# Performance work log

Hardware: AMD Instinct MI355X
Metric: run time of the kernel (lower is better)

The kernel has to match this reference:

```python
import jax, jax.numpy as jnp
import numpy as np

EPS = 1e-5

def _batchnorm(x, gamma, beta):
    # x: [N, C, T]; training-mode BN: batch stats over (N, T) per channel
    mean = jnp.mean(x, axis=(0, 2), keepdims=True)
    var = jnp.mean((x - mean) ** 2, axis=(0, 2), keepdims=True)
    xhat = (x - mean) * jax.lax.rsqrt(var + EPS)
    return xhat * gamma[None, :, None] + beta[None, :, None]

def _temporal_shift(x, s):
    # x: [N, C, T], s: [C] learnable per-channel shift (Shift-GCN style)
    # out[n,c,t] = linear interp of x[n,c, t + s[c]], zero outside [0, T)
    N, C, T = x.shape
    pos = jnp.arange(T, dtype=x.dtype)[None, :] + s[:, None]  # [C, T]
    i0f = jnp.floor(pos)
    frac = pos - i0f                                          # [C, T]
    i0 = i0f.astype(jnp.int32)
    i1 = i0 + 1
    v0 = ((i0 >= 0) & (i0 < T)).astype(x.dtype)
    v1 = ((i1 >= 0) & (i1 < T)).astype(x.dtype)
    cidx = jnp.arange(C)[:, None]                             # [C, 1]
    g0 = x[:, cidx, jnp.clip(i0, 0, T - 1)]                   # [N, C, T]
    g1 = x[:, cidx, jnp.clip(i1, 0, T - 1)]
    return g0 * ((1.0 - frac) * v0) + g1 * (frac * v1)

def setup_inputs() -> dict:
    key = jax.random.key(0)
    ks = jax.random.split(key, 5)
    N, T, Cin, Cout = 128, 1024, 256, 256
    x = jax.random.normal(ks[0], (N, T, Cin), dtype=jnp.float32)
    # kaiming_normal fan_out for 1x1 conv: std = sqrt(2 / Cout)
    conv_w = jax.random.normal(ks[1], (Cout, Cin), dtype=jnp.float32) * np.sqrt(2.0 / Cout)
    conv_b = jnp.zeros((Cout,), dtype=jnp.float32)
    shift_in_s = jax.random.uniform(ks[2], (Cin,), dtype=jnp.float32, minval=-1.0, maxval=1.0)
    shift_out_s = jax.random.uniform(ks[3], (Cout,), dtype=jnp.float32, minval=-1.0, maxval=1.0)
    return {
        "x": x,
        "bn1_gamma": jnp.ones((Cin,), jnp.float32),
        "bn1_beta": jnp.zeros((Cin,), jnp.float32),
        "shift_in_s": shift_in_s,
        "conv_w": conv_w,
        "conv_b": conv_b,
        "shift_out_s": shift_out_s,
        "bn2_gamma": jnp.ones((Cout,), jnp.float32),
        "bn2_beta": jnp.zeros((Cout,), jnp.float32),
    }

def reference(x, bn1_gamma, bn1_beta, shift_in_s, conv_w, conv_b, shift_out_s, bn2_gamma, bn2_beta):
    # x: [N, T, C] -> [N, C, T] (permute; trailing singleton W dim elided)
    h = jnp.transpose(x, (0, 2, 1))
    h = _batchnorm(h, bn1_gamma, bn1_beta)
    h = _temporal_shift(h, shift_in_s)
    # 1x1 conv == per-position channel mixing
    h = jnp.einsum("nct,oc->not", h, conv_w) + conv_b[None, :, None]
    h = jax.nn.relu(h)
    h = _temporal_shift(h, shift_out_s)
    h = _batchnorm(h, bn2_gamma, bn2_beta)
    return jnp.transpose(h, (0, 2, 1))  # back to [N, T, C_out]
```

## Files before the change

kernel.cpp:

```cpp
#include <hip/hip_runtime.h>
#include <stddef.h>

typedef __attribute__((ext_vector_type(8))) short short8;
typedef __attribute__((ext_vector_type(4))) float f32x4;
typedef __attribute__((ext_vector_type(4))) int   i32x4;
typedef __attribute__((ext_vector_type(2))) unsigned int u32x2;
typedef unsigned short ushort_t;
typedef unsigned int uint_t;

#define TT 1024
#define NT 131072.0f
#define EPS 1e-5f

__device__ __forceinline__ float bf2f(ushort_t u){
    union { float f; uint_t i; } v; v.i = ((uint_t)u) << 16; return v.f;
}
__device__ __forceinline__ ushort_t f2bf(float f){
    union { float f; uint_t i; } v; v.f = f;
    uint_t r = v.i + 0x7fffu + ((v.i >> 16) & 1u);
    return (ushort_t)(r >> 16);
}
__device__ __forceinline__ uint_t pack2(float lo, float hi){
    return (uint_t)f2bf(lo) | ((uint_t)f2bf(hi) << 16);
}
__device__ __forceinline__ f32x4 ld4bf(const ushort_t* p){
    u32x2 u = *(const u32x2*)p;
    f32x4 r;
    r[0] = bf2f((ushort_t)(u[0] & 0xffffu));
    r[1] = bf2f((ushort_t)(u[0] >> 16));
    r[2] = bf2f((ushort_t)(u[1] & 0xffffu));
    r[3] = bf2f((ushort_t)(u[1] >> 16));
    return r;
}
__device__ __forceinline__ void wave_red(float& v){
    #pragma unroll
    for (int off = 32; off > 0; off >>= 1) v += __shfl_down(v, off);
}

__global__ __launch_bounds__(256) void k_stats1(const float* __restrict__ x,
                                                ushort_t* __restrict__ xb16,
                                                float* __restrict__ psum,
                                                float* __restrict__ psq){
    __shared__ float ls[4][256], lq[4][256];
    const int b = blockIdx.x, tid = threadIdx.x;
    const int c4 = (tid & 63) << 2, rq = tid >> 6;
    const size_t row0 = ((size_t)b << 6) + ((size_t)rq << 4);
    const float* p = x + (row0 << 8) + c4;
    ushort_t* w = xb16 + (row0 << 8) + c4;
    f32x4 s = {0.f,0.f,0.f,0.f}, q = {0.f,0.f,0.f,0.f};
    #pragma unroll 8
    for (int k = 0; k < 16; ++k){
        f32x4 v = *(const f32x4*)&p[(size_t)k << 8];
        u32x2 u; u[0] = pack2(v[0], v[1]); u[1] = pack2(v[2], v[3]);
        *(u32x2*)&w[(size_t)k << 8] = u;
        #pragma unroll
        for (int j = 0; j < 4; ++j){ s[j] += v[j]; q[j] = fmaf(v[j], v[j], q[j]); }
    }
    #pragma unroll
    for (int j = 0; j < 4; ++j){ ls[rq][c4 + j] = s[j]; lq[rq][c4 + j] = q[j]; }
    __syncthreads();
    const int c = tid;
    psum[(size_t)b * 256 + c] = ls[0][c] + ls[1][c] + ls[2][c] + ls[3][c];
    psq [(size_t)b * 256 + c] = lq[0][c] + lq[1][c] + lq[2][c] + lq[3][c];
}

__global__ __launch_bounds__(256) void k_fin1(const float* __restrict__ psum,
                                              const float* __restrict__ psq,
                                              const float* __restrict__ g1,
                                              const float* __restrict__ be1,
                                              const float* __restrict__ sin_,
                                              const float* __restrict__ sout,
                                              float* __restrict__ s1, float* __restrict__ b1,
                                              float* __restrict__ a0i, float* __restrict__ a1i,
                                              int* __restrict__ i1i,
                                              float* __restrict__ a0o, float* __restrict__ a1o,
                                              int* __restrict__ j1o){
    const int c = blockIdx.x, t = threadIdx.x;
    float s = 0.f, q = 0.f;
    #pragma unroll
    for (int i = 0; i < 8; ++i){
        const size_t b = (size_t)(t * 8 + i);
        s += psum[b * 256 + c]; q += psq[b * 256 + c];
    }
    wave_red(s); wave_red(q);
    __shared__ float sm[8];
    const int wv = t >> 6, ln = t & 63;
    if (ln == 0){ sm[wv] = s; sm[4 + wv] = q; }
    __syncthreads();
    if (t == 0){
        float S = sm[0] + sm[1] + sm[2] + sm[3];
        float Q = sm[4] + sm[5] + sm[6] + sm[7];
        float mean = S / NT;
        float var  = Q / NT - mean * mean;
        float rstd = rsqrtf(var + EPS);
        float sc = rstd * g1[c];
        s1[c] = sc;
        b1[c] = be1[c] - mean * sc;
        float sv = sin_[c]; float fi = floorf(sv); float fr = sv - fi;
        a0i[c] = 1.f - fr; a1i[c] = fr; i1i[c] = (int)fi + 1;
        float so = sout[c]; float fo = floorf(so); float fro = so - fo;
        a0o[c] = 1.f - fro; a1o[c] = fro; j1o[c] = (int)fo + 1;
    }
}

__global__ __launch_bounds__(256) void k_wf(const float* __restrict__ W,
                                            const float* __restrict__ s1,
                                            ushort_t* __restrict__ WF){
    const int gid = blockIdx.x * 256 + threadIdx.x;
    const int l = gid & 63, ob = (gid >> 6) & 15, ks = gid >> 10;
    const int row = ob * 16 + (l & 15);
    const int k0  = ks * 32 + (l >> 4) * 8;
    #pragma unroll
    for (int j = 0; j < 8; ++j)
        WF[(size_t)gid * 8 + j] = f2bf(W[(size_t)row * 256 + k0 + j] * s1[k0 + j]);
}

__global__ __launch_bounds__(256) void k_wb(const float* __restrict__ W,
                                            const float* __restrict__ cb,
                                            const float* __restrict__ b1,
                                            const float* __restrict__ a0i,
                                            const float* __restrict__ a1i,
                                            const int* __restrict__ i1i,
                                            float* __restrict__ bias2,
                                            float* __restrict__ corr0,
                                            float* __restrict__ corrT){
    const int o = blockIdx.x, c = threadIdx.x;
    const float w = W[(size_t)o * 256 + c];
    float wb = w * b1[c];
    float c0 = (i1i[c] == 0) ? wb * a0i[c] : 0.f;
    float cT = (i1i[c] == 1) ? wb * a1i[c] : 0.f;
    wave_red(wb); wave_red(c0); wave_red(cT);
    __shared__ float sm[4][3];
    const int wv = c >> 6, ln = c & 63;
    if (ln == 0){ sm[wv][0] = wb; sm[wv][1] = c0; sm[wv][2] = cT; }
    __syncthreads();
    if (c == 0){
        bias2[o] = cb[o] + sm[0][0] + sm[1][0] + sm[2][0] + sm[3][0];
        corr0[o] = sm[0][1] + sm[1][1] + sm[2][1] + sm[3][1];
        corrT[o] = sm[0][2] + sm[1][2] + sm[2][2] + sm[3][2];
    }
}

__device__ __forceinline__ f32x4 bload16(const ushort_t* xp, int g){
    f32x4 r = {0.f,0.f,0.f,0.f};
    if (g >= 0 && g < TT) r = ld4bf(xp + ((size_t)g << 8));
    return r;
}

__global__ __launch_bounds__(256) void k_conv(const ushort_t* __restrict__ xb,
                                              const ushort_t* __restrict__ WF,
                                              const float* __restrict__ bias2,
                                              const float* __restrict__ corr0,
                                              const float* __restrict__ corrT,
                                              const float* __restrict__ a0i,
                                              const float* __restrict__ a1i,
                                              const int* __restrict__ i1i,
                                              ushort_t* __restrict__ Y,
                                              float* __restrict__ SP, float* __restrict__ SQ,
                                              float* __restrict__ SR,
                                              float* __restrict__ FR, float* __restrict__ LR){
    __shared__ __align__(16) ushort_t lds[16384];
    const int tid = threadIdx.x;
    const int n  = blockIdx.x >> 4;
    const int t0 = (blockIdx.x & 15) << 6;
    const int lane = tid & 63, wv = tid >> 6;

    {
        const int c4 = lane << 2;
        const f32x4 a0v = *(const f32x4*)&a0i[c4];
        const f32x4 a1v = *(const f32x4*)&a1i[c4];
        const i32x4 i1v = *(const i32x4*)&i1i[c4];
        const ushort_t* xp = xb + ((size_t)n << 18) + c4;
        const int rt = t0 + (wv << 4);
        f32x4 Bm1 = bload16(xp, rt - 1);
        f32x4 B0  = bload16(xp, rt);
        #pragma unroll 8
        for (int k = 0; k < 16; ++k){
            f32x4 Bp1 = bload16(xp, rt + k + 1);
            f32x4 v;
            #pragma unroll
            for (int j = 0; j < 4; ++j){
                float zl = i1v[j] ? B0[j]  : Bm1[j];
                float zr = i1v[j] ? Bp1[j] : B0[j];
                v[j] = a0v[j] * zl + a1v[j] * zr;
            }
            const int tw = (wv << 4) + k;
            u32x2 w; w[0] = pack2(v[0], v[1]); w[1] = pack2(v[2], v[3]);
            *(u32x2*)&lds[(tw << 8) + (c4 ^ ((tw & 7) << 3))] = w;
            Bm1 = B0; B0 = Bp1;
        }
    }
    __syncthreads();

    const int l15 = lane & 15, lg = lane >> 4;
    f32x4 acc[4][4];
    #pragma unroll
    for (int r = 0; r < 4; ++r)
        #pragma unroll
        for (int q = 0; q < 4; ++q)
            acc[r][q] = (f32x4){0.f, 0.f, 0.f, 0.f};

    const short8* wf8 = (const short8*)WF;
    #pragma unroll
    for (int ks = 0; ks < 8; ++ks){
        short8 aF[4], bF[4];
        #pragma unroll
        for (int r = 0; r < 4; ++r)
            aF[r] = wf8[(ks * 16 + wv * 4 + r) * 64 + lane];
        const int kk = (ks << 5) + (lg << 3);
        #pragma unroll
        for (int q = 0; q < 4; ++q){
            const int t = (q << 4) | l15;
            bF[q] = *(const short8*)&lds[(t << 8) + (kk ^ ((t & 7) << 3))];
        }
        #pragma unroll
        for (int r = 0; r < 4; ++r)
            #pragma unroll
            for (int q = 0; q < 4; ++q)
                acc[r][q] = __builtin_amdgcn_mfma_f32_16x16x32_bf16(aF[r], bF[q], acc[r][q], 0, 0, 0);
    }
    __syncthreads();

    const bool isFirst = (t0 == 0), isLast = (t0 == 960);
    #pragma unroll
    for (int r = 0; r < 4; ++r){
        const int ob = (wv << 6) + (r << 4) + (lg << 2);
        const f32x4 cbv = *(const f32x4*)&bias2[ob];
        f32x4 c0v = {0.f,0.f,0.f,0.f}, cTv = {0.f,0.f,0.f,0.f};
        if (isFirst) c0v = *(const f32x4*)&corr0[ob];
        if (isLast)  cTv = *(const f32x4*)&corrT[ob];
        #pragma unroll
        for (int q = 0; q < 4; ++q){
            const int t = (q << 4) | l15;
            float v[4];
            #pragma unroll
            for (int j = 0; j < 4; ++j){
                float z = acc[r][q][j] + cbv[j];
                if (isFirst && t == 0)  z -= c0v[j];
                if (isLast  && t == 63) z -= cTv[j];
                v[j] = z > 0.f ? z : 0.f;
            }
            u32x2 w; w[0] = pack2(v[0], v[1]); w[1] = pack2(v[2], v[3]);
            *(u32x2*)&lds[(t << 8) + (ob ^ ((t & 7) << 3))] = w;
        }
    }
    __syncthreads();

    u32x2* Yu = (u32x2*)Y;
    const size_t rbase = ((size_t)n << 10) + t0;
    #pragma unroll
    for (int it = 0; it < 16; ++it){
        const int row = (it << 2) + wv;
        u32x2 v = *(const u32x2*)&lds[(row << 8) + ((lane << 2) ^ ((row & 7) << 3))];
        Yu[((rbase + row) << 6) + lane] = v;
    }
    {
        const int o = tid;
        FR[(size_t)blockIdx.x * 256 + o] = bf2f(lds[o]);
        LR[(size_t)blockIdx.x * 256 + o] = bf2f(lds[(63 << 8) + (o ^ 56)]);
    }
    f32x4 P = {0.f,0.f,0.f,0.f}, Q = P, R = P;
    {
        const int o4 = lane << 2;
        const int r0 = wv << 4;
        f32x4 prev = {0.f,0.f,0.f,0.f};
        if (wv > 0) prev = ld4bf(&lds[((r0 - 1) << 8) + (o4 ^ (((r0 - 1) & 7) << 3))]);
        #pragma unroll 8
        for (int k = 0; k < 16; ++k){
            const int t = r0 + k;
            f32x4 y = ld4bf(&lds[(t << 8) + (o4 ^ ((t & 7) << 3))]);
            #pragma unroll
            for (int j = 0; j < 4; ++j){
                P[j] += y[j];
                Q[j] = fmaf(y[j], y[j], Q[j]);
                R[j] = fmaf(prev[j], y[j], R[j]);
            }
            prev = y;
        }
    }
    __syncthreads();
    float* fl = (float*)lds;
    {
        const int o4 = lane << 2;
        *(f32x4*)&fl[wv * 768 + o4]       = P;
        *(f32x4*)&fl[wv * 768 + 256 + o4] = Q;
        *(f32x4*)&fl[wv * 768 + 512 + o4] = R;
    }
    __syncthreads();
    {
        const int o = tid;
        float p = fl[o] + fl[768 + o] + fl[1536 + o] + fl[2304 + o];
        float q = fl[256 + o] + fl[1024 + o] + fl[1792 + o] + fl[2560 + o];
        float r = fl[512 + o] + fl[1280 + o] + fl[2048 + o] + fl[2816 + o];
        const size_t idx = (size_t)blockIdx.x * 256 + o;
        SP[idx] = p; SQ[idx] = q; SR[idx] = r;
    }
}

__global__ __launch_bounds__(256) void k_fin2(const float* __restrict__ SP,
                                              const float* __restrict__ SQ,
                                              const float* __restrict__ SR,
                                              const float* __restrict__ FR,
                                              const float* __restrict__ LR,
                                              const float* __restrict__ g2,
                                              const float* __restrict__ be2,
                                              const float* __restrict__ a0o,
                                              const float* __restrict__ a1o,
                                              const int* __restrict__ j1o,
                                              float* __restrict__ s2, float* __restrict__ b2){
    const int o = blockIdx.x, t = threadIdx.x;
    float P = 0.f, Q = 0.f, R = 0.f, b0p = 0.f, b0q = 0.f, btp = 0.f, btq = 0.f;
    #pragma unroll
    for (int i = 0; i < 8; ++i){
        const int b = t * 8 + i;
        const size_t idx = (size_t)b * 256 + o;
        P += SP[idx]; Q += SQ[idx];
        float r = SR[idx];
        const float fr = FR[idx], lr = LR[idx];
        const int tile = b & 15;
        if (tile > 0) r = fmaf(LR[idx - 256], fr, r);
        R += r;
        if (tile == 0){ b0p += fr; b0q += fr * fr; }
        if (tile == 15){ btp += lr; btq += lr * lr; }
    }
    wave_red(P); wave_red(Q); wave_red(R);
    wave_red(b0p); wave_red(b0q); wave_red(btp); wave_red(btq);
    __shared__ float sm[4][7];
    const int wv = t >> 6, ln = t & 63;
    if (ln == 0){
        sm[wv][0] = P; sm[wv][1] = Q; sm[wv][2] = R;
        sm[wv][3] = b0p; sm[wv][4] = b0q; sm[wv][5] = btp; sm[wv][6] = btq;
    }
    __syncthreads();
    if (t == 0){
        float v[7];
        #pragma unroll
        for (int k = 0; k < 7; ++k)
            v[k] = sm[0][k] + sm[1][k] + sm[2][k] + sm[3][k];
        const float a0 = a0o[o], a1 = a1o[o];
        const int j1 = j1o[o];
        float sz, sq;
        if (j1 == 0){
            sz = a0 * (v[0] - v[5]) + a1 * v[0];
            sq = a0 * a0 * (v[1] - v[6]) + a1 * a1 * v[1] + 2.f * a0 * a1 * v[2];
        } else {
            sz = a0 * v[0] + a1 * (v[0] - v[3]);
            sq = a0 * a0 * v[1] + a1 * a1 * (v[1] - v[4]) + 2.f * a0 * a1 * v[2];
        }
        float mean = sz / NT;
        float var  = sq / NT - mean * mean;
        float rstd = rsqrtf(var + EPS);
        float sc = rstd * g2[o];
        s2[o] = sc;
        b2[o] = be2[o] - mean * sc;
    }
}

__global__ __launch_bounds__(256) void k_out(const ushort_t* __restrict__ Y,
                                             const float* __restrict__ s2,
                                             const float* __restrict__ b2,
                                             const float* __restrict__ a0o,
                                             const float* __restrict__ a1o,
                                             const int* __restrict__ j1o,
                                             float* __restrict__ out){
    const int b = blockIdx.x, tid = threadIdx.x;
    const int n = b >> 3, o4 = (tid & 63) << 2, rq = tid >> 6;
    const int rs = ((b & 7) << 7) + (rq << 5);
    const f32x4 sc = *(const f32x4*)&s2[o4];
    const f32x4 bs = *(const f32x4*)&b2[o4];
    const f32x4 a0 = *(const f32x4*)&a0o[o4];
    const f32x4 a1 = *(const f32x4*)&a1o[o4];
    const i32x4 j1 = *(const i32x4*)&j1o[o4];
    const ushort_t* yb = Y + ((size_t)n << 18) + o4;
    float* ob = out + ((size_t)n << 18) + o4;
    f32x4 ym1 = {0.f,0.f,0.f,0.f};
    if (rs > 0) ym1 = ld4bf(yb + ((size_t)(rs - 1) << 8));
    f32x4 y0 = ld4bf(yb + ((size_t)rs << 8));
    #pragma unroll 8
    for (int k = 0; k < 32; ++k){
        const int t = rs + k;
        f32x4 yp1 = {0.f,0.f,0.f,0.f};
        if (t < 1023) yp1 = ld4bf(yb + ((size_t)(t + 1) << 8));
        f32x4 ov;
        #pragma unroll
        for (int j = 0; j < 4; ++j){
            float zl = j1[j] ? y0[j]  : ym1[j];
            float zr = j1[j] ? yp1[j] : y0[j];
            float z = a0[j] * zl + a1[j] * zr;
            ov[j] = fmaf(z, sc[j], bs[j]);
        }
        *(f32x4*)&ob[(size_t)t << 8] = ov;
        ym1 = y0; y0 = yp1;
    }
}

extern "C" void kernel_launch(void* const* d_in, const int* in_sizes, int n_in,
                              void* d_out, int out_size, void* d_ws, size_t ws_size,
                              hipStream_t stream){
    const float* x    = (const float*)d_in[0];
    const float* g1   = (const float*)d_in[1];
    const float* be1  = (const float*)d_in[2];
    const float* sin_ = (const float*)d_in[3];
    const float* W    = (const float*)d_in[4];
    const float* cb   = (const float*)d_in[5];
    const float* sout = (const float*)d_in[6];
    const float* g2   = (const float*)d_in[7];
    const float* be2  = (const float*)d_in[8];
    float* out = (float*)d_out;

    char* ws = (char*)d_ws;
    ushort_t* Y  = (ushort_t*)ws;
    ushort_t* WF = (ushort_t*)(ws + 67108864);
    float* SP = (float*)(ws + 67239936);
    float* SQ = SP + 524288;
    float* SR = SQ + 524288;
    float* FR = SR + 524288;
    float* LR = FR + 524288;
    float* par = LR + 524288;
    float* s1    = par;         float* b1    = par + 256;
    float* a0i   = par + 512;   float* a1i   = par + 768;
    int*   i1i   = (int*)(par + 1024);
    float* a0o   = par + 1280;  float* a1o   = par + 1536;
    int*   j1o   = (int*)(par + 1792);
    float* s2    = par + 2048;  float* b2    = par + 2304;
    float* bias2 = par + 2560;  float* corr0 = par + 2816;
    float* corrT = par + 3072;
    float* psum = (float*)ws;
    float* psq  = psum + 524288;
    ushort_t* xb16 = (ushort_t*)d_out;

    k_stats1<<<2048, 256, 0, stream>>>(x, xb16, psum, psq);
    k_fin1  <<<256, 256, 0, stream>>>(psum, psq, g1, be1, sin_, sout,
                                      s1, b1, a0i, a1i, i1i, a0o, a1o, j1o);
    k_wf    <<<32, 256, 0, stream>>>(W, s1, WF);
    k_wb    <<<256, 256, 0, stream>>>(W, cb, b1, a0i, a1i, i1i, bias2, corr0, corrT);
    k_conv  <<<2048, 256, 0, stream>>>(xb16, WF, bias2, corr0, corrT,
                                       a0i, a1i, i1i, Y, SP, SQ, SR, FR, LR);
    k_fin2  <<<256, 256, 0, stream>>>(SP, SQ, SR, FR, LR,
                                      g2, be2, a0o, a1o, j1o, s2, b2);
    k_out   <<<1024, 256, 0, stream>>>(Y, s2, b2, a0o, a1o, j1o, out);
}
```

Before: 168.9 us.

## Move input temporal shift into stats kernel and DMA pre-swizzled tile into LDS

The input-side temporal shift interpolation moves from the conv kernel's LDS staging into the first pass over x. That pass now writes a shifted, XOR-swizzled bf16 copy, so k_conv can fill LDS with direct global-to-LDS loads instead of register loads plus ALU work. The shift coefficients are computed in a new tiny kernel launched first, and k_out now uses twice as many blocks with half the rows each. This adds one launch and halo reads of neighbouring rows in the prep pass, in exchange for a leaner conv prologue.

```diff
diff --git a/kernel.cpp b/kernel.cpp
--- a/kernel.cpp
+++ b/kernel.cpp
@@ -36,25 +36,49 @@
     #pragma unroll
     for (int off = 32; off > 0; off >>= 1) v += __shfl_down(v, off);
 }
-
-__global__ __launch_bounds__(256) void k_stats1(const float* __restrict__ x,
-                                                ushort_t* __restrict__ xb16,
-                                                float* __restrict__ psum,
-                                                float* __restrict__ psq){
+__device__ __forceinline__ void dma16(const void* g, void* l){
+    __builtin_amdgcn_global_load_lds(
+        (const __attribute__((address_space(1))) unsigned int*)g,
+        (__attribute__((address_space(3))) unsigned int*)l, 16, 0, 0);
+}
+
+__global__ __launch_bounds__(256) void k_prep(const float* __restrict__ x,
+                                              const float* __restrict__ a0i,
+                                              const float* __restrict__ a1i,
+                                              const int* __restrict__ i1i,
+                                              ushort_t* __restrict__ xs,
+                                              float* __restrict__ psum,
+                                              float* __restrict__ psq){
     __shared__ float ls[4][256], lq[4][256];
     const int b = blockIdx.x, tid = threadIdx.x;
     const int c4 = (tid & 63) << 2, rq = tid >> 6;
     const size_t row0 = ((size_t)b << 6) + ((size_t)rq << 4);
-    const float* p = x + (row0 << 8) + c4;
-    ushort_t* w = xb16 + (row0 << 8) + c4;
+    const int n = (int)(row0 >> 10), rt = (int)(row0 & 1023);
+    const float* xp = x + ((size_t)n << 18) + c4;
+    ushort_t* wp = xs + ((size_t)n << 18);
+    const f32x4 a0v = *(const f32x4*)&a0i[c4];
+    const f32x4 a1v = *(const f32x4*)&a1i[c4];
+    const i32x4 i1v = *(const i32x4*)&i1i[c4];
     f32x4 s = {0.f,0.f,0.f,0.f}, q = {0.f,0.f,0.f,0.f};
+    f32x4 Bm1 = {0.f,0.f,0.f,0.f};
+    if (rt > 0) Bm1 = *(const f32x4*)&xp[(size_t)(rt - 1) << 8];
+    f32x4 B0 = *(const f32x4*)&xp[(size_t)rt << 8];
     #pragma unroll 8
     for (int k = 0; k < 16; ++k){
-        f32x4 v = *(const f32x4*)&p[(size_t)k << 8];
+        const int t = rt + k;
+        f32x4 Bp1 = {0.f,0.f,0.f,0.f};
+        if (t < 1023) Bp1 = *(const f32x4*)&xp[(size_t)(t + 1) << 8];
+        f32x4 v;
+        #pragma unroll
+        for (int j = 0; j < 4; ++j){
+            s[j] += B0[j]; q[j] = fmaf(B0[j], B0[j], q[j]);
+            float zl = i1v[j] ? B0[j]  : Bm1[j];
+            float zr = i1v[j] ? Bp1[j] : B0[j];
+            v[j] = a0v[j] * zl + a1v[j] * zr;
+        }
         u32x2 u; u[0] = pack2(v[0], v[1]); u[1] = pack2(v[2], v[3]);
-        *(u32x2*)&w[(size_t)k << 8] = u;
-        #pragma unroll
-        for (int j = 0; j < 4; ++j){ s[j] += v[j]; q[j] = fmaf(v[j], v[j], q[j]); }
+        *(u32x2*)&wp[((size_t)t << 8) + (c4 ^ ((t & 7) << 3))] = u;
+        Bm1 = B0; B0 = Bp1;
     }
     #pragma unroll
     for (int j = 0; j < 4; ++j){ ls[rq][c4 + j] = s[j]; lq[rq][c4 + j] = q[j]; }
@@ -62,19 +86,28 @@
     const int c = tid;
     psum[(size_t)b * 256 + c] = ls[0][c] + ls[1][c] + ls[2][c] + ls[3][c];
     psq [(size_t)b * 256 + c] = lq[0][c] + lq[1][c] + lq[2][c] + lq[3][c];
+}
+
+__global__ __launch_bounds__(256) void k_shift(const float* __restrict__ sin_,
+                                               const float* __restrict__ sout,
+                                               float* __restrict__ a0i, float* __restrict__ a1i,
+                                               int* __restrict__ i1i,
+                                               float* __restrict__ a0o, float* __restrict__ a1o,
+                                               int* __restrict__ j1o){
+    const int c = blockIdx.x * 256 + threadIdx.x;
+    if (c < 256){
+        float sv = sin_[c]; float fi = floorf(sv); float fr = sv - fi;
+        a0i[c] = 1.f - fr; a1i[c] = fr; i1i[c] = (int)fi + 1;
+        float so = sout[c]; float fo = floorf(so); float fro = so - fo;
+        a0o[c] = 1.f - fro; a1o[c] = fro; j1o[c] = (int)fo + 1;
+    }
 }
 
 __global__ __launch_bounds__(256) void k_fin1(const float* __restrict__ psum,
                                               const float* __restrict__ psq,
                                               const float* __restrict__ g1,
                                               const float* __restrict__ be1,
-                                              const float* __restrict__ sin_,
-                                              const float* __restrict__ sout,
-                                              float* __restrict__ s1, float* __restrict__ b1,
-                                              float* __restrict__ a0i, float* __restrict__ a1i,
-                                              int* __restrict__ i1i,
-                                              float* __restrict__ a0o, float* __restrict__ a1o,
-                                              int* __restrict__ j1o){
+                                              float* __restrict__ s1, float* __restrict__ b1){
     const int c = blockIdx.x, t = threadIdx.x;
     float s = 0.f, q = 0.f;
     #pragma unroll
@@ -96,10 +129,6 @@
         float sc = rstd * g1[c];
         s1[c] = sc;
         b1[c] = be1[c] - mean * sc;
-        float sv = sin_[c]; float fi = floorf(sv); float fr = sv - fi;
-        a0i[c] = 1.f - fr; a1i[c] = fr; i1i[c] = (int)fi + 1;
-        float so = sout[c]; float fo = floorf(so); float fro = so - fo;
-        a0o[c] = 1.f - fro; a1o[c] = fro; j1o[c] = (int)fo + 1;
     }
 }
 
@@ -141,20 +170,11 @@
     }
 }
 
-__device__ __forceinline__ f32x4 bload16(const ushort_t* xp, int g){
-    f32x4 r = {0.f,0.f,0.f,0.f};
-    if (g >= 0 && g < TT) r = ld4bf(xp + ((size_t)g << 8));
-    return r;
-}
-
-__global__ __launch_bounds__(256) void k_conv(const ushort_t* __restrict__ xb,
+__global__ __launch_bounds__(256) void k_conv(const ushort_t* __restrict__ xs,
                                               const ushort_t* __restrict__ WF,
                                               const float* __restrict__ bias2,
                                               const float* __restrict__ corr0,
                                               const float* __restrict__ corrT,
-                                              const float* __restrict__ a0i,
-                                              const float* __restrict__ a1i,
-                                              const int* __restrict__ i1i,
                                               ushort_t* __restrict__ Y,
                                               float* __restrict__ SP, float* __restrict__ SQ,
                                               float* __restrict__ SR,
@@ -166,29 +186,10 @@
     const int lane = tid & 63, wv = tid >> 6;
 
     {
-        const int c4 = lane << 2;
-        const f32x4 a0v = *(const f32x4*)&a0i[c4];
-        const f32x4 a1v = *(const f32x4*)&a1i[c4];
-        const i32x4 i1v = *(const i32x4*)&i1i[c4];
-        const ushort_t* xp = xb + ((size_t)n << 18) + c4;
-        const int rt = t0 + (wv << 4);
-        f32x4 Bm1 = bload16(xp, rt - 1);
-        f32x4 B0  = bload16(xp, rt);
-        #pragma unroll 8
-        for (int k = 0; k < 16; ++k){
-            f32x4 Bp1 = bload16(xp, rt + k + 1);
-            f32x4 v;
-            #pragma unroll
-            for (int j = 0; j < 4; ++j){
-                float zl = i1v[j] ? B0[j]  : Bm1[j];
-                float zr = i1v[j] ? Bp1[j] : B0[j];
-                v[j] = a0v[j] * zl + a1v[j] * zr;
-            }
-            const int tw = (wv << 4) + k;
-            u32x2 w; w[0] = pack2(v[0], v[1]); w[1] = pack2(v[2], v[3]);
-            *(u32x2*)&lds[(tw << 8) + (c4 ^ ((tw & 7) << 3))] = w;
-            Bm1 = B0; B0 = Bp1;
-        }
+        const ushort_t* gsrc = xs + ((size_t)n << 18) + ((size_t)(t0 + (wv << 4)) << 8);
+        #pragma unroll
+        for (int i = 0; i < 8; ++i)
+            dma16(gsrc + (i << 9) + (lane << 3), &lds[(wv << 12) + (i << 9)]);
     }
     __syncthreads();
 
@@ -364,8 +365,8 @@
                                              const int* __restrict__ j1o,
                                              float* __restrict__ out){
     const int b = blockIdx.x, tid = threadIdx.x;
-    const int n = b >> 3, o4 = (tid & 63) << 2, rq = tid >> 6;
-    const int rs = ((b & 7) << 7) + (rq << 5);
+    const int n = b >> 4, o4 = (tid & 63) << 2, rq = tid >> 6;
+    const int rs = ((b & 15) << 6) + (rq << 4);
     const f32x4 sc = *(const f32x4*)&s2[o4];
     const f32x4 bs = *(const f32x4*)&b2[o4];
     const f32x4 a0 = *(const f32x4*)&a0o[o4];
@@ -377,7 +378,7 @@
     if (rs > 0) ym1 = ld4bf(yb + ((size_t)(rs - 1) << 8));
     f32x4 y0 = ld4bf(yb + ((size_t)rs << 8));
     #pragma unroll 8
-    for (int k = 0; k < 32; ++k){
+    for (int k = 0; k < 16; ++k){
         const int t = rs + k;
         f32x4 yp1 = {0.f,0.f,0.f,0.f};
         if (t < 1023) yp1 = ld4bf(yb + ((size_t)(t + 1) << 8));
@@ -427,16 +428,16 @@
     float* corrT = par + 3072;
     float* psum = (float*)ws;
     float* psq  = psum + 524288;
-    ushort_t* xb16 = (ushort_t*)d_out;
-
-    k_stats1<<<2048, 256, 0, stream>>>(x, xb16, psum, psq);
-    k_fin1  <<<256, 256, 0, stream>>>(psum, psq, g1, be1, sin_, sout,
-                                      s1, b1, a0i, a1i, i1i, a0o, a1o, j1o);
-    k_wf    <<<32, 256, 0, stream>>>(W, s1, WF);
-    k_wb    <<<256, 256, 0, stream>>>(W, cb, b1, a0i, a1i, i1i, bias2, corr0, corrT);
-    k_conv  <<<2048, 256, 0, stream>>>(xb16, WF, bias2, corr0, corrT,
-                                       a0i, a1i, i1i, Y, SP, SQ, SR, FR, LR);
-    k_fin2  <<<256, 256, 0, stream>>>(SP, SQ, SR, FR, LR,
-                                      g2, be2, a0o, a1o, j1o, s2, b2);
-    k_out   <<<1024, 256, 0, stream>>>(Y, s2, b2, a0o, a1o, j1o, out);
-}
+    ushort_t* xs = (ushort_t*)d_out;
+
+    k_shift<<<1, 256, 0, stream>>>(sin_, sout, a0i, a1i, i1i, a0o, a1o, j1o);
+    k_prep <<<2048, 256, 0, stream>>>(x, a0i, a1i, i1i, xs, psum, psq);
+    k_fin1 <<<256, 256, 0, stream>>>(psum, psq, g1, be1, s1, b1);
+    k_wf   <<<32, 256, 0, stream>>>(W, s1, WF);
+    k_wb   <<<256, 256, 0, stream>>>(W, cb, b1, a0i, a1i, i1i, bias2, corr0, corrT);
+    k_conv <<<2048, 256, 0, stream>>>(xs, WF, bias2, corr0, corrT,
+                                      Y, SP, SQ, SR, FR, LR);
+    k_fin2 <<<256, 256, 0, stream>>>(SP, SQ, SR, FR, LR,
+                                     g2, be2, a0o, a1o, j1o, s2, b2);
+    k_out  <<<2048, 256, 0, stream>>>(Y, s2, b2, a0o, a1o, j1o, out);
+}
```

After: 162.2 us. -3.9%, faster.
